# Performance work log

Hardware: AMD Instinct MI355X
Metric: run time of the kernel (lower is better)

The kernel has to match this reference:

```python
import jax, jax.numpy as jnp
import numpy as np

DIM = 2048
N_HEADS = 16
HEAD_DIM = DIM // N_HEADS  # 128
MAX_LEN = 2048
B, T = 2, 2048
RESTORE_SCALE = DIM ** 0.5  # sqkinit / sqkscale = 1 / (1/sqrt(dim))
SQK_SCALE = 1.0 / DIM ** 0.5


def _rope_tables(seq_len, head_dim, dtype=jnp.float32):
    d2 = head_dim // 2
    pos = jnp.arange(seq_len, dtype=dtype)                     # [T]
    theta = 1.0 / (10000.0 ** (jnp.arange(0, head_dim, 2, dtype=dtype) / head_dim))  # [d2]
    ang = pos[:, None] * theta[None, :]                        # [T, d2]
    return jnp.cos(ang), jnp.sin(ang)


def _apply_rope(x, cos, sin):
    # x: [B, H, T, D]; cos/sin: [T, D/2] broadcast over B,H
    d2 = x.shape[-1] // 2
    xr, xi = x[..., :d2], x[..., d2:]
    return jnp.concatenate([xr * cos - xi * sin, xr * sin + xi * cos], axis=-1)


def setup_inputs() -> dict:
    key = jax.random.key(0)
    ks = jax.random.split(key, 5)
    s = 0.02
    return {
        "x":  jax.random.normal(ks[0], (B, T, DIM), jnp.float32),
        "Wq": jax.random.normal(ks[1], (DIM, DIM), jnp.float32) * s,
        "Wk": jax.random.normal(ks[2], (DIM, DIM), jnp.float32) * s,
        "Wv": jax.random.normal(ks[3], (DIM, DIM), jnp.float32) * s,
        "Wo": jax.random.normal(ks[4], (DIM, DIM), jnp.float32) * s,
        "sqk": jnp.ones((N_HEADS, 1, HEAD_DIM), jnp.float32) * SQK_SCALE,
    }


def reference(x, Wq, Wk, Wv, Wo, sqk):
    Bc, Tc, C = x.shape
    # QKV projections (torch Linear: x @ W.T), split heads -> [B, H, T, D]
    def proj(W):
        return (x @ W.T).reshape(Bc, Tc, N_HEADS, HEAD_DIM).transpose(0, 2, 1, 3)
    q, k, v = proj(Wq), proj(Wk), proj(Wv)

    cos, sin = _rope_tables(Tc, HEAD_DIM, x.dtype)
    actual_sqk = sqk * RESTORE_SCALE  # [H, 1, D]
    q = _apply_rope(q, cos, sin) * actual_sqk
    k = _apply_rope(k, cos, sin) * actual_sqk

    # SDPA with scale = sqrt(head_dim) (as in the source, not 1/sqrt)
    scale = HEAD_DIM ** 0.5
    scores = jnp.einsum("bhtd,bhsd->bhts", q, k) * scale  # [B, H, T, T]
    causal = jnp.tril(jnp.ones((Tc, Tc), bool))
    scores = jnp.where(causal, scores, -jnp.inf)
    attn = jax.nn.softmax(scores, axis=-1)
    out = jnp.einsum("bhts,bhsd->bhtd", attn, v)           # [B, H, T, D]
    out = out.transpose(0, 2, 1, 3).reshape(Bc, Tc, C)

    y = out @ Wo.T
    # F.normalize(p=2, dim=-1, eps=1e-12)
    norm = jnp.linalg.norm(y, axis=-1, keepdims=True)
    return y / jnp.maximum(norm, 1e-12)
```

## Files before the change

kernel.cpp:

```cpp
#include <hip/hip_runtime.h>

#define DEVFN __device__ __forceinline__

typedef float    floatx4 __attribute__((ext_vector_type(4)));
typedef _Float16 half8   __attribute__((ext_vector_type(8)));
typedef _Float16 half4v  __attribute__((ext_vector_type(4)));

#define MFMA16H(a, b, c) __builtin_amdgcn_mfma_f32_16x16x32_f16((a), (b), (c), 0, 0, 0)

DEVFN void async16(void* lds, const void* g) {
  __builtin_amdgcn_global_load_lds(
      (const __attribute__((address_space(1))) unsigned int*)g,
      (__attribute__((address_space(3))) unsigned int*)lds, 16, 0, 0);
}
DEVFN half8 ld8h(const _Float16* p) { return *(const half8*)p; }

__global__ __launch_bounds__(256) void cvt_prep(
    const float4* __restrict__ x, const float4* __restrict__ wq,
    const float4* __restrict__ wk, const float4* __restrict__ wv,
    const float4* __restrict__ wo,
    half4v* __restrict__ xh, half4v* __restrict__ xl,
    half4v* __restrict__ qo, half4v* __restrict__ ko,
    half4v* __restrict__ vo, half4v* __restrict__ oo,
    float* __restrict__ cosT, float* __restrict__ sinT) {
  int i = blockIdx.x * 256 + threadIdx.x;
  {
    float4 v = x[i];
    half4v h = {(_Float16)v.x, (_Float16)v.y, (_Float16)v.z, (_Float16)v.w};
    half4v l = {(_Float16)(v.x - (float)h.x), (_Float16)(v.y - (float)h.y),
                (_Float16)(v.z - (float)h.z), (_Float16)(v.w - (float)h.w)};
    xh[i] = h;
    xl[i] = l;
  }
  if (i < 1048576) {
    float4 v = wq[i];
    qo[i] = (half4v){(_Float16)v.x, (_Float16)v.y, (_Float16)v.z, (_Float16)v.w};
    v = wk[i];
    ko[i] = (half4v){(_Float16)v.x, (_Float16)v.y, (_Float16)v.z, (_Float16)v.w};
    v = wv[i];
    vo[i] = (half4v){(_Float16)v.x, (_Float16)v.y, (_Float16)v.z, (_Float16)v.w};
    v = wo[i];
    oo[i] = (half4v){(_Float16)v.x, (_Float16)v.y, (_Float16)v.z, (_Float16)v.w};
  }
  if (i < 131072) {
    int t = i >> 6, d = i & 63;
    double theta = exp(-((double)(2 * d) / 128.0) * log(10000.0));
    double ang = (double)t * theta;
    cosT[i] = (float)cos(ang);
    sinT[i] = (float)sin(ang);
  }
}

__global__ __launch_bounds__(512, 2) void gemm_qk_f16(
    const _Float16* __restrict__ xhp, const _Float16* __restrict__ xlp,
    const _Float16* __restrict__ wqp, const _Float16* __restrict__ wkp,
    const float* __restrict__ cosT, const float* __restrict__ sinT,
    const float* __restrict__ sqk,
    _Float16* __restrict__ qhi, _Float16* __restrict__ qlo,
    _Float16* __restrict__ khi) {
  constexpr int Kd = 2048, NT = 64;
  const int n0 = blockIdx.x * 128, m0 = blockIdx.y * 256;
  const int tid = threadIdx.x, w = tid >> 6, lane = tid & 63;
  const int quad = lane >> 4, l16 = lane & 15;
  const int c0 = w & 1, rb = w >> 1, rgb = rb * 4;
  const int cgr0 = 2 * c0, cgr1 = 2 * c0 + 1, cgr2 = 2 * c0 + 4, cgr3 = 2 * c0 + 5;

  __shared__ __align__(16) _Float16 smem[57344];
  _Float16* XH = smem;
  _Float16* XL = smem + 16384;
  _Float16* WQ = smem + 32768;
  _Float16* WK = smem + 45056;

  floatx4 accQ[4][4], accK[4][4];
#pragma unroll
  for (int i = 0; i < 4; i++)
#pragma unroll
    for (int c = 0; c < 4; c++) {
      accQ[i][c] = (floatx4){0.f, 0.f, 0.f, 0.f};
      accK[i][c] = (floatx4){0.f, 0.f, 0.f, 0.f};
    }

  const size_t xg0 = (size_t)(m0 + 32 * w + l16) * Kd + quad * 8;
  const size_t xg1 = xg0 + (size_t)16 * Kd;
  const size_t wg = (size_t)(n0 + 16 * w + l16) * Kd + quad * 8;

#define STAGE_X(T)                                                      \
  {                                                                     \
    const int kk_ = (T) * 32;                                           \
    _Float16* bx_ = XH + ((T) & 1) * 8192;                              \
    _Float16* bl_ = XL + ((T) & 1) * 8192;                              \
    async16(bx_ + (2 * w) * 512, xhp + xg0 + kk_);                      \
    async16(bx_ + (2 * w + 1) * 512, xhp + xg1 + kk_);                  \
    async16(bl_ + (2 * w) * 512, xlp + xg0 + kk_);                      \
    async16(bl_ + (2 * w + 1) * 512, xlp + xg1 + kk_);                  \
  }
#define STAGE_W(T)                                                      \
  {                                                                     \
    const int kk_ = (T) * 32;                                           \
    async16(WQ + ((T) % 3) * 4096 + w * 512, wqp + wg + kk_);           \
    async16(WK + ((T) % 3) * 4096 + w * 512, wkp + wg + kk_);           \
  }

  STAGE_X(0);
  STAGE_W(0);
  STAGE_W(1);
  asm volatile("s_waitcnt vmcnt(2)" ::: "memory");
  __builtin_amdgcn_s_barrier();
  __builtin_amdgcn_sched_barrier(0);

#pragma unroll 1
  for (int t = 0; t < NT; ++t) {
    const _Float16* XH_ = XH + (t & 1) * 8192;
    const _Float16* XL_ = XL + (t & 1) * 8192;
    const _Float16* WQ_ = WQ + (t % 3) * 4096;
    const _Float16* WK_ = WK + (t % 3) * 4096;

    half8 ah[4], al[4], bq[4], bk[4];
#pragma unroll
    for (int i = 0; i < 4; i++) {
      ah[i] = ld8h(XH_ + (rgb + i) * 512 + lane * 8);
      al[i] = ld8h(XL_ + (rgb + i) * 512 + lane * 8);
    }
    bq[0] = ld8h(WQ_ + cgr0 * 512 + lane * 8);
    bq[1] = ld8h(WQ_ + cgr1 * 512 + lane * 8);
    bq[2] = ld8h(WQ_ + cgr2 * 512 + lane * 8);
    bq[3] = ld8h(WQ_ + cgr3 * 512 + lane * 8);
    bk[0] = ld8h(WK_ + cgr0 * 512 + lane * 8);
    bk[1] = ld8h(WK_ + cgr1 * 512 + lane * 8);
    bk[2] = ld8h(WK_ + cgr2 * 512 + lane * 8);
    bk[3] = ld8h(WK_ + cgr3 * 512 + lane * 8);
    if (t + 1 < NT) STAGE_X(t + 1);
    if (t + 2 < NT) STAGE_W(t + 2);
    __builtin_amdgcn_s_setprio(1);
#pragma unroll
    for (int i = 0; i < 4; i++)
#pragma unroll
      for (int c = 0; c < 4; c++)
        accQ[i][c] = MFMA16H(ah[i], bq[c], accQ[i][c]);
#pragma unroll
    for (int i = 0; i < 4; i++)
#pragma unroll
      for (int c = 0; c < 4; c++)
        accQ[i][c] = MFMA16H(al[i], bq[c], accQ[i][c]);
#pragma unroll
    for (int i = 0; i < 4; i++)
#pragma unroll
      for (int c = 0; c < 4; c++)
        accK[i][c] = MFMA16H(ah[i], bk[c], accK[i][c]);
#pragma unroll
    for (int i = 0; i < 4; i++)
#pragma unroll
      for (int c = 0; c < 4; c++)
        accK[i][c] = MFMA16H(al[i], bk[c], accK[i][c]);
    __builtin_amdgcn_s_setprio(0);

    if (t + 2 < NT) {
      asm volatile("s_waitcnt vmcnt(2)" ::: "memory");
    } else {
      asm volatile("s_waitcnt vmcnt(0)" ::: "memory");
    }
    __builtin_amdgcn_s_barrier();
    __builtin_amdgcn_sched_barrier(0);
  }
#undef STAGE_X
#undef STAGE_W

  __syncthreads();
  _Float16* stH = smem + w * 1152;
  _Float16* stL = smem + 9216 + w * 1152;

  const int h = n0 >> 7;
  const int b = m0 >> 11;

#pragma unroll
  for (int rg = 0; rg < 4; rg++) {
    const int tt0 = (m0 & 2047) + rb * 64 + rg * 16;
    const size_t gbase = (((size_t)(b * 16 + h)) * 2048 + tt0) * 128;

#pragma unroll
    for (int cj = 0; cj < 2; cj++) {
      int d = c0 * 32 + cj * 16 + l16;
      float s1 = sqk[h * 128 + d] * 512.0f;
      float s2 = sqk[h * 128 + d + 64] * 512.0f;
#pragma unroll
      for (int r = 0; r < 4; r++) {
        int tq = tt0 + quad * 4 + r;
        float cc = cosT[tq * 64 + d], sn = sinT[tq * 64 + d];
        float xr = accQ[rg][cj][r], xi = accQ[rg][cj + 2][r];
        float o1 = (xr * cc - xi * sn) * s1;
        float o2 = (xr * sn + xi * cc) * s2;
        _Float16 h1 = (_Float16)o1, h2 = (_Float16)o2;
        int rl = quad * 4 + r;
        stH[rl * 72 + cj * 16 + l16] = h1;
        stH[rl * 72 + 32 + cj * 16 + l16] = h2;
        stL[rl * 72 + cj * 16 + l16] = (_Float16)(o1 - (float)h1);
        stL[rl * 72 + 32 + cj * 16 + l16] = (_Float16)(o2 - (float)h2);
      }
    }
#pragma unroll
    for (int it = 0; it < 2; it++) {
      int row = it * 8 + (lane >> 3), pc = (lane & 7) * 8;
      int d = (pc < 32) ? (c0 * 32 + pc) : (64 + c0 * 32 + (pc - 32));
      size_t ga = gbase + (size_t)row * 128 + d;
      *(half8*)(qhi + ga) = ld8h(&stH[row * 72 + pc]);
      *(half8*)(qlo + ga) = ld8h(&stL[row * 72 + pc]);
    }

#pragma unroll
    for (int cj = 0; cj < 2; cj++) {
      int d = c0 * 32 + cj * 16 + l16;
      float s1 = sqk[h * 128 + d] * 45.254834f;
      float s2 = sqk[h * 128 + d + 64] * 45.254834f;
#pragma unroll
      for (int r = 0; r < 4; r++) {
        int tq = tt0 + quad * 4 + r;
        float cc = cosT[tq * 64 + d], sn = sinT[tq * 64 + d];
        float xr = accK[rg][cj][r], xi = accK[rg][cj + 2][r];
        int rl = quad * 4 + r;
        stH[rl * 72 + cj * 16 + l16] = (_Float16)((xr * cc - xi * sn) * s1);
        stH[rl * 72 + 32 + cj * 16 + l16] = (_Float16)((xr * sn + xi * cc) * s2);
      }
    }
#pragma unroll
    for (int it = 0; it < 2; it++) {
      int row = it * 8 + (lane >> 3), pc = (lane & 7) * 8;
      int d = (pc < 32) ? (c0 * 32 + pc) : (64 + c0 * 32 + (pc - 32));
      *(half8*)(khi + gbase + (size_t)row * 128 + d) = ld8h(&stH[row * 72 + pc]);
    }
  }
}

__global__ __launch_bounds__(512, 2) void gemm_v_f16(
    const _Float16* __restrict__ xhp, const _Float16* __restrict__ wvp,
    _Float16* __restrict__ vt) {
  constexpr int Kd = 2048, NT = 64;
  const int n0 = blockIdx.x * 128, m0 = blockIdx.y * 256;
  const int tid = threadIdx.x, w = tid >> 6, lane = tid & 63;
  const int quad = lane >> 4, l16 = lane & 15;
  const int c0 = w & 1, rb = w >> 1, rgb = rb * 4;

  __shared__ __align__(16) _Float16 smem[28672];
  _Float16* XH = smem;
  _Float16* WV = smem + 16384;

  floatx4 accV[4][4];
#pragma unroll
  for (int i = 0; i < 4; i++)
#pragma unroll
    for (int c = 0; c < 4; c++) accV[i][c] = (floatx4){0.f, 0.f, 0.f, 0.f};

  const size_t xg0 = (size_t)(m0 + 32 * w + l16) * Kd + quad * 8;
  const size_t xg1 = xg0 + (size_t)16 * Kd;
  const size_t wg = (size_t)(n0 + 16 * w + l16) * Kd + quad * 8;

#define STAGE_XV(T)                                                     \
  {                                                                     \
    const int kk_ = (T) * 32;                                           \
    _Float16* bx_ = XH + ((T) & 1) * 8192;                              \
    async16(bx_ + (2 * w) * 512, xhp + xg0 + kk_);                      \
    async16(bx_ + (2 * w + 1) * 512, xhp + xg1 + kk_);                  \
  }
#define STAGE_WV(T)                                                     \
  { async16(WV + ((T) % 3) * 4096 + w * 512, wvp + wg + (T) * 32); }

  STAGE_XV(0);
  STAGE_WV(0);
  STAGE_WV(1);
  asm volatile("s_waitcnt vmcnt(1)" ::: "memory");
  __builtin_amdgcn_s_barrier();
  __builtin_amdgcn_sched_barrier(0);

#pragma unroll 1
  for (int t = 0; t < NT; ++t) {
    const _Float16* XH_ = XH + (t & 1) * 8192;
    const _Float16* WV_ = WV + (t % 3) * 4096;

    half8 ah[4], bv[4];
#pragma unroll
    for (int i = 0; i < 4; i++)
      ah[i] = ld8h(XH_ + (rgb + i) * 512 + lane * 8);
#pragma unroll
    for (int c = 0; c < 4; c++)
      bv[c] = ld8h(WV_ + (4 * c0 + c) * 512 + lane * 8);
    if (t + 1 < NT) STAGE_XV(t + 1);
    if (t + 2 < NT) STAGE_WV(t + 2);
    __builtin_amdgcn_s_setprio(1);
#pragma unroll
    for (int i = 0; i < 4; i++)
#pragma unroll
      for (int c = 0; c < 4; c++)
        accV[i][c] = MFMA16H(ah[i], bv[c], accV[i][c]);
    __builtin_amdgcn_s_setprio(0);
    if (t + 2 < NT) {
      asm volatile("s_waitcnt vmcnt(1)" ::: "memory");
    } else {
      asm volatile("s_waitcnt vmcnt(0)" ::: "memory");
    }
    __builtin_amdgcn_s_barrier();
    __builtin_amdgcn_sched_barrier(0);
  }
#undef STAGE_XV
#undef STAGE_WV

  __syncthreads();
  _Float16* stV = smem + w * 1024;

  const int h = n0 >> 7;
  const int b = m0 >> 11;
  const int bh = b * 16 + h;

#pragma unroll
  for (int rg = 0; rg < 4; rg++) {
    const int tt0 = (m0 & 2047) + rb * 64 + rg * 16;
#pragma unroll
    for (int c = 0; c < 4; c++)
#pragma unroll
      for (int r = 0; r < 4; r++)
        stV[(c * 16 + l16) * 16 + quad * 4 + r] = (_Float16)accV[rg][c][r];
#pragma unroll
    for (int it = 0; it < 2; it++) {
      int dl = it * 32 + (lane >> 1), th = (lane & 1) * 8;
      int dh = c0 * 64 + dl;
      size_t ga = ((size_t)bh * 128 + dh) * 2048 + tt0 + th;
      *(half8*)(vt + ga) = ld8h(&stV[dl * 16 + th]);
    }
  }
}

__global__ __launch_bounds__(256, 2) void flash_attn(
    const _Float16* __restrict__ qhp, const _Float16* __restrict__ qlp,
    const _Float16* __restrict__ khp,
    const _Float16* __restrict__ vtp, _Float16* __restrict__ aout) {
  constexpr int T = 2048, HD = 128;
  const int bh = blockIdx.x;
  const int qt = 31 - blockIdx.y;
  const int q0 = qt * 64;
  const int tid = threadIdx.x, w = tid >> 6, lane = tid & 63;
  const int quad = lane >> 4, l16 = lane & 15;

  __shared__ __align__(16) _Float16 Kh[2][8192];
  __shared__ __align__(16) _Float16 Vt[2][8192];
  __shared__ __align__(16) _Float16 Pb[4][16 * 72];

  const size_t qkbase = (size_t)bh * T * HD;
  const size_t vbase = (size_t)bh * HD * T;

  auto stageKV = [&](int kt, int set) {
    const int s0 = kt * 64;
    for (int c = w; c < 16; c += 4) {
      int tt = c >> 2, ss = c & 3;
      size_t go = qkbase + (size_t)(s0 + tt * 16 + l16) * HD + ss * 32 + quad * 8;
      async16(&Kh[set][c * 512], khp + go);
      int dt = c >> 1, vs = c & 1;
      size_t vo = vbase + (size_t)(dt * 16 + l16) * T + s0 + vs * 32 + quad * 8;
      async16(&Vt[set][c * 512], vtp + vo);
    }
  };

  half8 qh[4], ql[4];
#pragma unroll
  for (int s = 0; s < 4; s++) {
    size_t off = qkbase + (size_t)(q0 + w * 16 + l16) * HD + s * 32 + quad * 8;
    qh[s] = *(const half8*)(qhp + off);
    ql[s] = *(const half8*)(qlp + off);
  }

  floatx4 o[8];
#pragma unroll
  for (int dt = 0; dt < 8; dt++) o[dt] = (floatx4){0.f, 0.f, 0.f, 0.f};
  float mrow[4], lrow[4];
#pragma unroll
  for (int r = 0; r < 4; r++) { mrow[r] = -3e38f; lrow[r] = 0.f; }

  const int ntiles = qt + 1;

  stageKV(0, 0);
  __syncthreads();

#pragma unroll 1
  for (int kt = 0; kt < ntiles; ++kt) {
    const int s0 = kt * 64;
    const int set = kt & 1;
    if (kt + 1 < ntiles) stageKV(kt + 1, set ^ 1);

    floatx4 S[4];
#pragma unroll
    for (int j = 0; j < 4; j++) S[j] = (floatx4){0.f, 0.f, 0.f, 0.f};

    __builtin_amdgcn_s_setprio(1);
#pragma unroll
    for (int s = 0; s < 4; s++) {
#pragma unroll
      for (int j = 0; j < 4; j++) {
        half8 kh = ld8h(&Kh[set][(j * 4 + s) * 512 + lane * 8]);
        S[j] = MFMA16H(qh[s], kh, S[j]);
        S[j] = MFMA16H(ql[s], kh, S[j]);
      }
    }
    __builtin_amdgcn_s_setprio(0);

    if (kt == ntiles - 1) {
      int rbase = q0 + w * 16 + quad * 4;
#pragma unroll
      for (int j = 0; j < 4; j++) {
        int cg = s0 + j * 16 + l16;
#pragma unroll
        for (int r = 0; r < 4; r++)
          if (cg > rbase + r) S[j][r] = -3e38f;
      }
    }

    float lm[4];
#pragma unroll
    for (int r = 0; r < 4; r++)
      lm[r] = fmaxf(fmaxf(S[0][r], S[1][r]), fmaxf(S[2][r], S[3][r]));

    bool ok = true;
#pragma unroll
    for (int r = 0; r < 4; r++) ok = ok && (lm[r] <= mrow[r] + 8.0f);

    if (!__all(ok ? 1 : 0)) {
#pragma unroll
      for (int d = 1; d < 16; d <<= 1)
#pragma unroll
        for (int r = 0; r < 4; r++)
          lm[r] = fmaxf(lm[r], __shfl_xor(lm[r], d, 64));
#pragma unroll
      for (int r = 0; r < 4; r++) {
        float mnew = fmaxf(mrow[r], lm[r]);
        float al = __expf(mrow[r] - mnew);
        mrow[r] = mnew;
        lrow[r] *= al;
#pragma unroll
        for (int dt = 0; dt < 8; dt++) o[dt][r] *= al;
      }
    }

    float rs[4];
#pragma unroll
    for (int r = 0; r < 4; r++) {
      float e0 = __expf(S[0][r] - mrow[r]);
      float e1 = __expf(S[1][r] - mrow[r]);
      float e2 = __expf(S[2][r] - mrow[r]);
      float e3 = __expf(S[3][r] - mrow[r]);
      S[0][r] = e0; S[1][r] = e1; S[2][r] = e2; S[3][r] = e3;
      rs[r] = (e0 + e1) + (e2 + e3);
    }
#pragma unroll
    for (int d = 1; d < 16; d <<= 1)
#pragma unroll
      for (int r = 0; r < 4; r++) rs[r] += __shfl_xor(rs[r], d, 64);
#pragma unroll
    for (int r = 0; r < 4; r++) lrow[r] += rs[r];

    half8 pf[2];
#pragma unroll
    for (int r = 0; r < 4; r++)
#pragma unroll
      for (int j = 0; j < 4; j++)
        Pb[w][(quad * 4 + r) * 72 + j * 16 + l16] = (_Float16)S[j][r];
    pf[0] = ld8h(&Pb[w][l16 * 72 + quad * 8]);
    pf[1] = ld8h(&Pb[w][l16 * 72 + 32 + quad * 8]);

    __builtin_amdgcn_s_setprio(1);
#pragma unroll
    for (int dt = 0; dt < 8; dt++) {
#pragma unroll
      for (int s = 0; s < 2; s++) {
        half8 vf = ld8h(&Vt[set][(dt * 2 + s) * 512 + lane * 8]);
        o[dt] = MFMA16H(pf[s], vf, o[dt]);
      }
    }
    __builtin_amdgcn_s_setprio(0);
    __syncthreads();
  }

  const int b = bh >> 4, h = bh & 15;
#pragma unroll
  for (int r = 0; r < 4; r++) {
    int trow = q0 + w * 16 + quad * 4 + r;
    float linv = 1.0f / lrow[r];
    size_t base = ((size_t)(b * T + trow)) * 2048 + h * 128;
#pragma unroll
    for (int dt = 0; dt < 8; dt++)
      aout[base + dt * 16 + l16] = (_Float16)(o[dt][r] * linv);
  }
}

__global__ __launch_bounds__(512, 2) void gemm_o_f16(
    const _Float16* __restrict__ A, const _Float16* __restrict__ Bw,
    float* __restrict__ outF) {
  constexpr int Kd = 2048, NT = 64;
  const int n0 = blockIdx.x * 128, m0 = blockIdx.y * 256;
  const int tid = threadIdx.x, w = tid >> 6, lane = tid & 63;
  const int quad = lane >> 4, l16 = lane & 15;
  const int c0 = w & 1, rb = w >> 1, rgb = rb * 4;

  __shared__ __align__(16) _Float16 smem[28672];
  _Float16* AH = smem;
  _Float16* WB = smem + 16384;

  floatx4 acc[4][4];
#pragma unroll
  for (int i = 0; i < 4; i++)
#pragma unroll
    for (int c = 0; c < 4; c++) acc[i][c] = (floatx4){0.f, 0.f, 0.f, 0.f};

  const size_t ag0 = (size_t)(m0 + 32 * w + l16) * Kd + quad * 8;
  const size_t ag1 = ag0 + (size_t)16 * Kd;
  const size_t wg = (size_t)(n0 + 16 * w + l16) * Kd + quad * 8;

#define STAGE_A(T)                                                      \
  {                                                                     \
    const int kk_ = (T) * 32;                                           \
    _Float16* b_ = AH + ((T) & 1) * 8192;                               \
    async16(b_ + (2 * w) * 512, A + ag0 + kk_);                         \
    async16(b_ + (2 * w + 1) * 512, A + ag1 + kk_);                     \
  }
#define STAGE_B(T)                                                      \
  { async16(WB + ((T) % 3) * 4096 + w * 512, Bw + wg + (T) * 32); }

  STAGE_A(0);
  STAGE_B(0);
  STAGE_B(1);
  asm volatile("s_waitcnt vmcnt(1)" ::: "memory");
  __builtin_amdgcn_s_barrier();
  __builtin_amdgcn_sched_barrier(0);

#pragma unroll 1
  for (int t = 0; t < NT; ++t) {
    const _Float16* AH_ = AH + (t & 1) * 8192;
    const _Float16* WB_ = WB + (t % 3) * 4096;

    half8 a[4], b[4];
#pragma unroll
    for (int i = 0; i < 4; i++)
      a[i] = ld8h(AH_ + (rgb + i) * 512 + lane * 8);
#pragma unroll
    for (int c = 0; c < 4; c++)
      b[c] = ld8h(WB_ + (4 * c0 + c) * 512 + lane * 8);
    if (t + 1 < NT) STAGE_A(t + 1);
    if (t + 2 < NT) STAGE_B(t + 2);
    __builtin_amdgcn_s_setprio(1);
#pragma unroll
    for (int i = 0; i < 4; i++)
#pragma unroll
      for (int c = 0; c < 4; c++)
        acc[i][c] = MFMA16H(a[i], b[c], acc[i][c]);
    __builtin_amdgcn_s_setprio(0);
    if (t + 2 < NT) {
      asm volatile("s_waitcnt vmcnt(1)" ::: "memory");
    } else {
      asm volatile("s_waitcnt vmcnt(0)" ::: "memory");
    }
    __builtin_amdgcn_s_barrier();
    __builtin_amdgcn_sched_barrier(0);
  }
#undef STAGE_A
#undef STAGE_B

#pragma unroll
  for (int i = 0; i < 4; i++) {
    int rbase = m0 + (rgb + i) * 16 + quad * 4;
#pragma unroll
    for (int c = 0; c < 4; c++) {
      int col = n0 + (4 * c0 + c) * 16 + l16;
#pragma unroll
      for (int r = 0; r < 4; r++)
        outF[(size_t)(rbase + r) * 2048 + col] = acc[i][c][r];
    }
  }
}

__global__ __launch_bounds__(256) void rownorm(const float* __restrict__ y,
                                               float* __restrict__ out) {
  int row = blockIdx.x;
  const float4* yr = (const float4*)(y + (size_t)row * 2048);
  float4* od = (float4*)(out + (size_t)row * 2048);
  int t = threadIdx.x;
  float4 v0 = yr[t], v1 = yr[t + 256];
  float ss = v0.x * v0.x + v0.y * v0.y + v0.z * v0.z + v0.w * v0.w +
             v1.x * v1.x + v1.y * v1.y + v1.z * v1.z + v1.w * v1.w;
#pragma unroll
  for (int d = 1; d < 64; d <<= 1) ss += __shfl_xor(ss, d, 64);
  __shared__ float red[4];
  if ((t & 63) == 0) red[t >> 6] = ss;
  __syncthreads();
  float tot = red[0] + red[1] + red[2] + red[3];
  float inv = 1.0f / fmaxf(sqrtf(tot), 1e-12f);
  v0.x *= inv; v0.y *= inv; v0.z *= inv; v0.w *= inv;
  v1.x *= inv; v1.y *= inv; v1.z *= inv; v1.w *= inv;
  od[t] = v0;
  od[t + 256] = v1;
}

extern "C" void kernel_launch(void* const* d_in, const int* in_sizes, int n_in,
                              void* d_out, int out_size, void* d_ws, size_t ws_size,
                              hipStream_t stream) {
  (void)in_sizes; (void)n_in; (void)out_size; (void)ws_size;
  const float* x   = (const float*)d_in[0];
  const float* Wq  = (const float*)d_in[1];
  const float* Wk  = (const float*)d_in[2];
  const float* Wv  = (const float*)d_in[3];
  const float* Wo  = (const float*)d_in[4];
  const float* sqk = (const float*)d_in[5];
  char* ws = (char*)d_ws;

  constexpr size_t SZX = 8388608ull * 2;
  constexpr size_t SZW = 4194304ull * 2;

  size_t o_xh = 0;
  size_t o_xl = o_xh + SZX;
  size_t o_wq = o_xl + SZX;
  size_t o_wk = o_wq + SZW;
  size_t o_wv = o_wk + SZW;
  size_t o_wo = o_wv + SZW;
  size_t o_qh = o_wo + SZW;
  size_t o_ql = o_qh + SZX;
  size_t o_kh = o_ql + SZX;
  size_t o_v  = o_kh + SZX;
  size_t o_vt = o_v + SZX;
  size_t o_cos = o_vt + SZX;
  size_t o_sin = o_cos + 2048 * 64 * 4;
  size_t o_aout = o_wq;
  size_t o_y    = o_qh;

  _Float16* xh = (_Float16*)(ws + o_xh);
  _Float16* xl = (_Float16*)(ws + o_xl);
  _Float16* wq = (_Float16*)(ws + o_wq);
  _Float16* wk = (_Float16*)(ws + o_wk);
  _Float16* wv = (_Float16*)(ws + o_wv);
  _Float16* wo = (_Float16*)(ws + o_wo);
  _Float16* qh = (_Float16*)(ws + o_qh);
  _Float16* ql = (_Float16*)(ws + o_ql);
  _Float16* kh = (_Float16*)(ws + o_kh);
  _Float16* vt = (_Float16*)(ws + o_vt);
  float* cosT = (float*)(ws + o_cos);
  float* sinT = (float*)(ws + o_sin);
  _Float16* aout = (_Float16*)(ws + o_aout);
  float* y = (float*)(ws + o_y);

  cvt_prep<<<8192, 256, 0, stream>>>((const float4*)x, (const float4*)Wq,
                                     (const float4*)Wk, (const float4*)Wv,
                                     (const float4*)Wo, (half4v*)xh, (half4v*)xl,
                                     (half4v*)wq, (half4v*)wk, (half4v*)wv,
                                     (half4v*)wo, cosT, sinT);

  gemm_qk_f16<<<dim3(16, 16), 512, 0, stream>>>(xh, xl, wq, wk, cosT, sinT,
                                                sqk, qh, ql, kh);
  gemm_v_f16<<<dim3(16, 16), 512, 0, stream>>>(xh, wv, vt);

  flash_attn<<<dim3(32, 32), 256, 0, stream>>>(qh, ql, kh, vt, aout);

  gemm_o_f16<<<dim3(16, 16), 512, 0, stream>>>(aout, wo, y);
  rownorm<<<4096, 256, 0, stream>>>(y, (float*)d_out);
}
```

Before: 500.8 us.

## Split QK projection k-step into four barrier-separated MFMA phases with interleaved loads

Restructures the Q/K projection inner loop into four phases, each loading only two B fragments from LDS and issuing 16 MFMAs, with workgroup barriers between phases so waves alternate between load and compute. The Wq and Wk global-to-LDS stages are split and issued in different phases to spread memory traffic. This lowers register pressure from the B fragments and aims to overlap waves' MFMA bursts with other waves' LDS reads. It adds many extra s_barrier instructions per iteration and removes the sched_barriers, which could add synchronization overhead.

```diff
diff --git a/kernel.cpp b/kernel.cpp
--- a/kernel.cpp
+++ b/kernel.cpp
@@ -94,19 +94,18 @@
     async16(bl_ + (2 * w) * 512, xlp + xg0 + kk_);                      \
     async16(bl_ + (2 * w + 1) * 512, xlp + xg1 + kk_);                  \
   }
-#define STAGE_W(T)                                                      \
-  {                                                                     \
-    const int kk_ = (T) * 32;                                           \
-    async16(WQ + ((T) % 3) * 4096 + w * 512, wqp + wg + kk_);           \
-    async16(WK + ((T) % 3) * 4096 + w * 512, wkp + wg + kk_);           \
-  }
+#define STAGE_WQ(T)                                                     \
+  { async16(WQ + ((T) % 3) * 4096 + w * 512, wqp + wg + (T) * 32); }
+#define STAGE_WK(T)                                                     \
+  { async16(WK + ((T) % 3) * 4096 + w * 512, wkp + wg + (T) * 32); }
 
   STAGE_X(0);
-  STAGE_W(0);
-  STAGE_W(1);
+  STAGE_WQ(0);
+  STAGE_WK(0);
+  STAGE_WQ(1);
+  STAGE_WK(1);
   asm volatile("s_waitcnt vmcnt(2)" ::: "memory");
   __builtin_amdgcn_s_barrier();
-  __builtin_amdgcn_sched_barrier(0);
 
 #pragma unroll 1
   for (int t = 0; t < NT; ++t) {
@@ -115,43 +114,89 @@
     const _Float16* WQ_ = WQ + (t % 3) * 4096;
     const _Float16* WK_ = WK + (t % 3) * 4096;
 
-    half8 ah[4], al[4], bq[4], bk[4];
+    half8 ah[4], al[4], b0, b1;
+
 #pragma unroll
     for (int i = 0; i < 4; i++) {
       ah[i] = ld8h(XH_ + (rgb + i) * 512 + lane * 8);
       al[i] = ld8h(XL_ + (rgb + i) * 512 + lane * 8);
     }
-    bq[0] = ld8h(WQ_ + cgr0 * 512 + lane * 8);
-    bq[1] = ld8h(WQ_ + cgr1 * 512 + lane * 8);
-    bq[2] = ld8h(WQ_ + cgr2 * 512 + lane * 8);
-    bq[3] = ld8h(WQ_ + cgr3 * 512 + lane * 8);
-    bk[0] = ld8h(WK_ + cgr0 * 512 + lane * 8);
-    bk[1] = ld8h(WK_ + cgr1 * 512 + lane * 8);
-    bk[2] = ld8h(WK_ + cgr2 * 512 + lane * 8);
-    bk[3] = ld8h(WK_ + cgr3 * 512 + lane * 8);
+    b0 = ld8h(WQ_ + cgr0 * 512 + lane * 8);
+    b1 = ld8h(WQ_ + cgr1 * 512 + lane * 8);
     if (t + 1 < NT) STAGE_X(t + 1);
-    if (t + 2 < NT) STAGE_W(t + 2);
+    __builtin_amdgcn_s_barrier();
+    asm volatile("s_waitcnt lgkmcnt(0)");
+    __builtin_amdgcn_sched_barrier(0);
     __builtin_amdgcn_s_setprio(1);
 #pragma unroll
-    for (int i = 0; i < 4; i++)
-#pragma unroll
-      for (int c = 0; c < 4; c++)
-        accQ[i][c] = MFMA16H(ah[i], bq[c], accQ[i][c]);
-#pragma unroll
-    for (int i = 0; i < 4; i++)
-#pragma unroll
-      for (int c = 0; c < 4; c++)
-        accQ[i][c] = MFMA16H(al[i], bq[c], accQ[i][c]);
-#pragma unroll
-    for (int i = 0; i < 4; i++)
-#pragma unroll
-      for (int c = 0; c < 4; c++)
-        accK[i][c] = MFMA16H(ah[i], bk[c], accK[i][c]);
-#pragma unroll
-    for (int i = 0; i < 4; i++)
-#pragma unroll
-      for (int c = 0; c < 4; c++)
-        accK[i][c] = MFMA16H(al[i], bk[c], accK[i][c]);
+    for (int i = 0; i < 4; i++) {
+      accQ[i][0] = MFMA16H(ah[i], b0, accQ[i][0]);
+      accQ[i][1] = MFMA16H(ah[i], b1, accQ[i][1]);
+    }
+#pragma unroll
+    for (int i = 0; i < 4; i++) {
+      accQ[i][0] = MFMA16H(al[i], b0, accQ[i][0]);
+      accQ[i][1] = MFMA16H(al[i], b1, accQ[i][1]);
+    }
+    __builtin_amdgcn_s_setprio(0);
+    __builtin_amdgcn_s_barrier();
+
+    b0 = ld8h(WQ_ + cgr2 * 512 + lane * 8);
+    b1 = ld8h(WQ_ + cgr3 * 512 + lane * 8);
+    if (t + 2 < NT) STAGE_WQ(t + 2);
+    __builtin_amdgcn_s_barrier();
+    asm volatile("s_waitcnt lgkmcnt(0)");
+    __builtin_amdgcn_sched_barrier(0);
+    __builtin_amdgcn_s_setprio(1);
+#pragma unroll
+    for (int i = 0; i < 4; i++) {
+      accQ[i][2] = MFMA16H(ah[i], b0, accQ[i][2]);
+      accQ[i][3] = MFMA16H(ah[i], b1, accQ[i][3]);
+    }
+#pragma unroll
+    for (int i = 0; i < 4; i++) {
+      accQ[i][2] = MFMA16H(al[i], b0, accQ[i][2]);
+      accQ[i][3] = MFMA16H(al[i], b1, accQ[i][3]);
+    }
+    __builtin_amdgcn_s_setprio(0);
+    __builtin_amdgcn_s_barrier();
+
+    b0 = ld8h(WK_ + cgr0 * 512 + lane * 8);
+    b1 = ld8h(WK_ + cgr1 * 512 + lane * 8);
+    __builtin_amdgcn_s_barrier();
+    asm volatile("s_waitcnt lgkmcnt(0)");
+    __builtin_amdgcn_sched_barrier(0);
+    __builtin_amdgcn_s_setprio(1);
+#pragma unroll
+    for (int i = 0; i < 4; i++) {
+      accK[i][0] = MFMA16H(ah[i], b0, accK[i][0]);
+      accK[i][1] = MFMA16H(ah[i], b1, accK[i][1]);
+    }
+#pragma unroll
+    for (int i = 0; i < 4; i++) {
+      accK[i][0] = MFMA16H(al[i], b0, accK[i][0]);
+      accK[i][1] = MFMA16H(al[i], b1, accK[i][1]);
+    }
+    __builtin_amdgcn_s_setprio(0);
+    __builtin_amdgcn_s_barrier();
+
+    b0 = ld8h(WK_ + cgr2 * 512 + lane * 8);
+    b1 = ld8h(WK_ + cgr3 * 512 + lane * 8);
+    if (t + 2 < NT) STAGE_WK(t + 2);
+    __builtin_amdgcn_s_barrier();
+    asm volatile("s_waitcnt lgkmcnt(0)");
+    __builtin_amdgcn_sched_barrier(0);
+    __builtin_amdgcn_s_setprio(1);
+#pragma unroll
+    for (int i = 0; i < 4; i++) {
+      accK[i][2] = MFMA16H(ah[i], b0, accK[i][2]);
+      accK[i][3] = MFMA16H(ah[i], b1, accK[i][3]);
+    }
+#pragma unroll
+    for (int i = 0; i < 4; i++) {
+      accK[i][2] = MFMA16H(al[i], b0, accK[i][2]);
+      accK[i][3] = MFMA16H(al[i], b1, accK[i][3]);
+    }
     __builtin_amdgcn_s_setprio(0);
 
     if (t + 2 < NT) {
@@ -160,10 +205,10 @@
       asm volatile("s_waitcnt vmcnt(0)" ::: "memory");
     }
     __builtin_amdgcn_s_barrier();
-    __builtin_amdgcn_sched_barrier(0);
   }
 #undef STAGE_X
-#undef STAGE_W
+#undef STAGE_WQ
+#undef STAGE_WK
 
   __syncthreads();
   _Float16* stH = smem + w * 1152;
```

New measurement: 498.9 us. No clear change (-0.4%).

## Load QK GEMM weight fragments directly from global into registers, bypassing LDS

Applied to the files above, without the earlier changes.

The Q/K projection GEMM no longer stages Wq/Wk tiles through a triple-buffered LDS ring. Each wave now loads its B-operand fragments straight from global memory into double-buffered registers one K-step ahead, with the loop unrolled by two to ping-pong the buffers. This drops the LDS reads and writes for the weights and shrinks shared memory, which could help occupancy. In exchange, the two waves sharing a column group fetch the same weight rows redundantly from global/L2, and more global-load latency must be hidden by register prefetch.

```diff
diff --git a/kernel.cpp b/kernel.cpp
--- a/kernel.cpp
+++ b/kernel.cpp
@@ -63,13 +63,10 @@
   const int tid = threadIdx.x, w = tid >> 6, lane = tid & 63;
   const int quad = lane >> 4, l16 = lane & 15;
   const int c0 = w & 1, rb = w >> 1, rgb = rb * 4;
-  const int cgr0 = 2 * c0, cgr1 = 2 * c0 + 1, cgr2 = 2 * c0 + 4, cgr3 = 2 * c0 + 5;
-
-  __shared__ __align__(16) _Float16 smem[57344];
+
+  __shared__ __align__(16) _Float16 smem[32768];
   _Float16* XH = smem;
   _Float16* XL = smem + 16384;
-  _Float16* WQ = smem + 32768;
-  _Float16* WK = smem + 45056;
 
   floatx4 accQ[4][4], accK[4][4];
 #pragma unroll
@@ -82,7 +79,8 @@
 
   const size_t xg0 = (size_t)(m0 + 32 * w + l16) * Kd + quad * 8;
   const size_t xg1 = xg0 + (size_t)16 * Kd;
-  const size_t wg = (size_t)(n0 + 16 * w + l16) * Kd + quad * 8;
+  const _Float16* wqb = wqp + (size_t)(n0 + 32 * c0 + l16) * Kd + quad * 8;
+  const _Float16* wkb = wkp + (size_t)(n0 + 32 * c0 + l16) * Kd + quad * 8;
 
 #define STAGE_X(T)                                                      \
   {                                                                     \
@@ -94,76 +92,94 @@
     async16(bl_ + (2 * w) * 512, xlp + xg0 + kk_);                      \
     async16(bl_ + (2 * w + 1) * 512, xlp + xg1 + kk_);                  \
   }
-#define STAGE_W(T)                                                      \
-  {                                                                     \
-    const int kk_ = (T) * 32;                                           \
-    async16(WQ + ((T) % 3) * 4096 + w * 512, wqp + wg + kk_);           \
-    async16(WK + ((T) % 3) * 4096 + w * 512, wkp + wg + kk_);           \
-  }
+
+  half8 bqA[4], bkA[4], bqB[4], bkB[4];
 
   STAGE_X(0);
-  STAGE_W(0);
-  STAGE_W(1);
-  asm volatile("s_waitcnt vmcnt(2)" ::: "memory");
+  __builtin_amdgcn_sched_barrier(0);
+  bqA[0] = ld8h(wqb);
+  bqA[1] = ld8h(wqb + 32768);
+  bqA[2] = ld8h(wqb + 131072);
+  bqA[3] = ld8h(wqb + 163840);
+  bkA[0] = ld8h(wkb);
+  bkA[1] = ld8h(wkb + 32768);
+  bkA[2] = ld8h(wkb + 131072);
+  bkA[3] = ld8h(wkb + 163840);
+  __builtin_amdgcn_sched_barrier(0);
+  asm volatile("s_waitcnt vmcnt(8)" ::: "memory");
   __builtin_amdgcn_s_barrier();
   __builtin_amdgcn_sched_barrier(0);
 
+#define QK_STEP(T, BQ, BK, BQN, BKN)                                    \
+  {                                                                     \
+    const _Float16* XH_ = XH + ((T) & 1) * 8192;                        \
+    const _Float16* XL_ = XL + ((T) & 1) * 8192;                        \
+    half8 ah[4], al[4];                                                 \
+    _Pragma("unroll")                                                   \
+    for (int i = 0; i < 4; i++) {                                       \
+      ah[i] = ld8h(XH_ + (rgb + i) * 512 + lane * 8);                   \
+      al[i] = ld8h(XL_ + (rgb + i) * 512 + lane * 8);                   \
+    }                                                                   \
+    if ((T) + 1 < NT) STAGE_X((T) + 1);                                 \
+    __builtin_amdgcn_sched_barrier(0);                                  \
+    if ((T) + 1 < NT) {                                                 \
+      const int kc_ = ((T) + 1) * 32;                                   \
+      BQN[0] = ld8h(wqb + kc_);                                         \
+      BQN[1] = ld8h(wqb + 32768 + kc_);                                 \
+      BQN[2] = ld8h(wqb + 131072 + kc_);                                \
+      BQN[3] = ld8h(wqb + 163840 + kc_);                                \
+      BKN[0] = ld8h(wkb + kc_);                                         \
+      BKN[1] = ld8h(wkb + 32768 + kc_);                                 \
+      BKN[2] = ld8h(wkb + 131072 + kc_);                                \
+      BKN[3] = ld8h(wkb + 163840 + kc_);                                \
+    }                                                                   \
+    __builtin_amdgcn_sched_barrier(0);                                  \
+    __builtin_amdgcn_s_setprio(1);                                      \
+    _Pragma("unroll")                                                   \
+    for (int i = 0; i < 4; i++) {                                       \
+      accQ[i][0] = MFMA16H(ah[i], BQ[0], accQ[i][0]);                   \
+      accQ[i][1] = MFMA16H(ah[i], BQ[1], accQ[i][1]);                   \
+      accQ[i][2] = MFMA16H(ah[i], BQ[2], accQ[i][2]);                   \
+      accQ[i][3] = MFMA16H(ah[i], BQ[3], accQ[i][3]);                   \
+    }                                                                   \
+    _Pragma("unroll")                                                   \
+    for (int i = 0; i < 4; i++) {                                       \
+      accQ[i][0] = MFMA16H(al[i], BQ[0], accQ[i][0]);                   \
+      accQ[i][1] = MFMA16H(al[i], BQ[1], accQ[i][1]);                   \
+      accQ[i][2] = MFMA16H(al[i], BQ[2], accQ[i][2]);                   \
+      accQ[i][3] = MFMA16H(al[i], BQ[3], accQ[i][3]);                   \
+    }                                                                   \
+    _Pragma("unroll")                                                   \
+    for (int i = 0; i < 4; i++) {                                       \
+      accK[i][0] = MFMA16H(ah[i], BK[0], accK[i][0]);                   \
+      accK[i][1] = MFMA16H(ah[i], BK[1], accK[i][1]);                   \
+      accK[i][2] = MFMA16H(ah[i], BK[2], accK[i][2]);                   \
+      accK[i][3] = MFMA16H(ah[i], BK[3], accK[i][3]);                   \
+    }                                                                   \
+    _Pragma("unroll")                                                   \
+    for (int i = 0; i < 4; i++) {                                       \
+      accK[i][0] = MFMA16H(al[i], BK[0], accK[i][0]);                   \
+      accK[i][1] = MFMA16H(al[i], BK[1], accK[i][1]);                   \
+      accK[i][2] = MFMA16H(al[i], BK[2], accK[i][2]);                   \
+      accK[i][3] = MFMA16H(al[i], BK[3], accK[i][3]);                   \
+    }                                                                   \
+    __builtin_amdgcn_s_setprio(0);                                      \
+    if ((T) + 1 < NT) {                                                 \
+      asm volatile("s_waitcnt vmcnt(8)" ::: "memory");                  \
+    } else {                                                            \
+      asm volatile("s_waitcnt vmcnt(0)" ::: "memory");                  \
+    }                                                                   \
+    __builtin_amdgcn_s_barrier();                                       \
+    __builtin_amdgcn_sched_barrier(0);                                  \
+  }
+
 #pragma unroll 1
-  for (int t = 0; t < NT; ++t) {
-    const _Float16* XH_ = XH + (t & 1) * 8192;
-    const _Float16* XL_ = XL + (t & 1) * 8192;
-    const _Float16* WQ_ = WQ + (t % 3) * 4096;
-    const _Float16* WK_ = WK + (t % 3) * 4096;
-
-    half8 ah[4], al[4], bq[4], bk[4];
-#pragma unroll
-    for (int i = 0; i < 4; i++) {
-      ah[i] = ld8h(XH_ + (rgb + i) * 512 + lane * 8);
-      al[i] = ld8h(XL_ + (rgb + i) * 512 + lane * 8);
-    }
-    bq[0] = ld8h(WQ_ + cgr0 * 512 + lane * 8);
-    bq[1] = ld8h(WQ_ + cgr1 * 512 + lane * 8);
-    bq[2] = ld8h(WQ_ + cgr2 * 512 + lane * 8);
-    bq[3] = ld8h(WQ_ + cgr3 * 512 + lane * 8);
-    bk[0] = ld8h(WK_ + cgr0 * 512 + lane * 8);
-    bk[1] = ld8h(WK_ + cgr1 * 512 + lane * 8);
-    bk[2] = ld8h(WK_ + cgr2 * 512 + lane * 8);
-    bk[3] = ld8h(WK_ + cgr3 * 512 + lane * 8);
-    if (t + 1 < NT) STAGE_X(t + 1);
-    if (t + 2 < NT) STAGE_W(t + 2);
-    __builtin_amdgcn_s_setprio(1);
-#pragma unroll
-    for (int i = 0; i < 4; i++)
-#pragma unroll
-      for (int c = 0; c < 4; c++)
-        accQ[i][c] = MFMA16H(ah[i], bq[c], accQ[i][c]);
-#pragma unroll
-    for (int i = 0; i < 4; i++)
-#pragma unroll
-      for (int c = 0; c < 4; c++)
-        accQ[i][c] = MFMA16H(al[i], bq[c], accQ[i][c]);
-#pragma unroll
-    for (int i = 0; i < 4; i++)
-#pragma unroll
-      for (int c = 0; c < 4; c++)
-        accK[i][c] = MFMA16H(ah[i], bk[c], accK[i][c]);
-#pragma unroll
-    for (int i = 0; i < 4; i++)
-#pragma unroll
-      for (int c = 0; c < 4; c++)
-        accK[i][c] = MFMA16H(al[i], bk[c], accK[i][c]);
-    __builtin_amdgcn_s_setprio(0);
-
-    if (t + 2 < NT) {
-      asm volatile("s_waitcnt vmcnt(2)" ::: "memory");
-    } else {
-      asm volatile("s_waitcnt vmcnt(0)" ::: "memory");
-    }
-    __builtin_amdgcn_s_barrier();
-    __builtin_amdgcn_sched_barrier(0);
-  }
+  for (int tt = 0; tt < NT; tt += 2) {
+    QK_STEP(tt, bqA, bkA, bqB, bkB);
+    QK_STEP(tt + 1, bqB, bkB, bqA, bkA);
+  }
+#undef QK_STEP
 #undef STAGE_X
-#undef STAGE_W
 
   __syncthreads();
   _Float16* stH = smem + w * 1152;
```

After: 717.9 us. +43.4%, slower.
